# Optimization experiments

Measured on AMD Instinct MI355X. Metric: run time of the kernel, lower is better.

The kernel has to match this reference:

```python
import jax, jax.numpy as jnp
import numpy as np

B, T, N, L, D, F = 8, 1024, 512, 4096, 512, 64  # batch, target, nodes, leaves, d_model, d_feature
BR = L // N  # branching factor: leaves per node


def setup_inputs() -> dict:
    key = jax.random.key(0)
    ks = jax.random.split(key, 10)
    s = 0.02
    return {
        "root": jax.random.normal(ks[0], (B, 1, F), dtype=jnp.float32),
        "node": jax.random.normal(ks[1], (B, N, D), dtype=jnp.float32),
        "leaf": jax.random.normal(ks[2], (B, L, D), dtype=jnp.float32),
        "target": jax.random.normal(ks[3], (B, T, D), dtype=jnp.float32),
        "Wq": jax.random.normal(ks[4], (D, F), dtype=jnp.float32) * s,
        "bq": jnp.zeros((F,), dtype=jnp.float32),
        "Wk": jax.random.normal(ks[5], (D, F), dtype=jnp.float32) * s,
        "bk": jnp.zeros((F,), dtype=jnp.float32),
        "Wv": jax.random.normal(ks[6], (D, F), dtype=jnp.float32) * s,
        "bv": jnp.zeros((F,), dtype=jnp.float32),
        "Wagg": jax.random.normal(ks[7], (D, 1), dtype=jnp.float32) * s,
        "bagg": jnp.zeros((1,), dtype=jnp.float32),
    }


def reference(root, node, leaf, target, Wq, bq, Wk, bk, Wv, bv, Wagg, bagg):
    # Shared DecoderLinear projections (same weights used for node and leaf).
    q = target @ Wq + bq                      # [B,T,F]
    node_k = node @ Wk + bk                   # [B,N,F]
    node_v = node @ Wv + bv                   # [B,N,F]
    leaf_k = leaf @ Wk + bk                   # [B,L,F]
    leaf_v = leaf @ Wv + bv                   # [B,L,F]

    scale = 1.0 / jnp.sqrt(jnp.asarray(F, dtype=q.dtype))
    # Dual-key attention weights (no value-matmul inside attention()).
    Aqn = jax.nn.softmax(jnp.einsum('btf,bnf->btn', q, node_k) * scale, axis=-1)  # [B,T,N]
    Aql = jax.nn.softmax(jnp.einsum('btf,blf->btl', q, leaf_k) * scale, axis=-1)  # [B,T,L]

    # Tree interpolation: each leaf mixes root, its parent node value, and itself.
    node_rep = jnp.repeat(node_v, BR, axis=1)               # [B,L,F]
    interp = (root + node_rep + leaf_v) / 3.0               # [B,L,F]

    # Upward cumulative aggregation: suffix mean along the leaf dimension.
    rev_cumsum = jnp.cumsum(interp[:, ::-1, :], axis=1)[:, ::-1, :]  # [B,L,F]
    counts = (L - jnp.arange(L)).astype(interp.dtype)[None, :, None]
    upward = rev_cumsum / counts                                     # [B,L,F]

    # Weighted aggregation: learned softmax weights over each node's leaf group.
    w = jax.nn.softmax((leaf @ Wagg + bagg).reshape(B, N, BR), axis=-1)   # [B,N,BR]
    node_hat = jnp.einsum('bnc,bncf->bnf', w, upward.reshape(B, N, BR, F))  # [B,N,F]

    # Fused cat + matmul + softmax.
    A = jnp.concatenate([Aqn, Aql], axis=-1)          # [B,T,N+L]
    V = jnp.concatenate([node_hat, leaf_v], axis=-2)  # [B,N+L,F]
    return jax.nn.softmax(jnp.einsum('btm,bmf->btf', A, V), axis=-1)  # [B,T,F]
```

## Files before the change

kernel.cpp:

```cpp
#include <hip/hip_runtime.h>

#define B_ 8
#define T_ 1024
#define N_ 512
#define L_ 4096
#define D_ 512
#define F_ 64
#define SLICES 8
#define TPS 9
#define KSTR 72
#define XSTR 520

typedef __attribute__((ext_vector_type(8))) short short8;
typedef __attribute__((ext_vector_type(4))) float f32x4;

__device__ __forceinline__ unsigned short f2bf(float x){
    unsigned u = __builtin_bit_cast(unsigned, x);
    u += 0x7FFFu + ((u >> 16) & 1u);
    return (unsigned short)(u >> 16);
}
__device__ __forceinline__ unsigned pack_bf(float lo, float hi){
    return (unsigned)f2bf(lo) | ((unsigned)f2bf(hi) << 16);
}
__device__ __forceinline__ float bf2f(unsigned short s){
    return __builtin_bit_cast(float, ((unsigned)s) << 16);
}
__device__ __forceinline__ short8 frag_from4(unsigned d0, unsigned d1, unsigned d2, unsigned d3){
    union { unsigned u[4]; short8 s; } t;
    t.u[0] = d0; t.u[1] = d1; t.u[2] = d2; t.u[3] = d3;
    return t.s;
}

__global__ __launch_bounds__(64)
void prep_kernel(const float* __restrict__ Wq, const float* __restrict__ bq,
                 const float* __restrict__ Wk, const float* __restrict__ bk,
                 const float* __restrict__ Wv, const float* __restrict__ bv,
                 unsigned short* __restrict__ Wq_t, unsigned short* __restrict__ Wkv_t,
                 float* __restrict__ bq_s, float* __restrict__ bkv)
{
    const int n = blockIdx.x;
    const int lane = threadIdx.x;
    if (n == 192) {
        bq_s[lane]   = bq[lane] * 0.125f;
        bkv[lane]    = bk[lane];
        bkv[64+lane] = bv[lane];
        return;
    }
    const int d0 = lane * 8;
    unsigned short t[8];
    if (n < 64) {
        #pragma unroll
        for (int j = 0; j < 8; ++j) t[j] = f2bf(Wq[(size_t)(d0+j)*F_ + n] * 0.125f);
        *(uint4*)&Wq_t[(size_t)n*D_ + d0] = make_uint4(
            (unsigned)t[0]|((unsigned)t[1]<<16), (unsigned)t[2]|((unsigned)t[3]<<16),
            (unsigned)t[4]|((unsigned)t[5]<<16), (unsigned)t[6]|((unsigned)t[7]<<16));
    } else {
        const int nn  = n - 64;
        const float* W = (nn < 64) ? Wk : Wv;
        const int col = nn & 63;
        #pragma unroll
        for (int j = 0; j < 8; ++j) t[j] = f2bf(W[(size_t)(d0+j)*F_ + col]);
        *(uint4*)&Wkv_t[(size_t)nn*D_ + d0] = make_uint4(
            (unsigned)t[0]|((unsigned)t[1]<<16), (unsigned)t[2]|((unsigned)t[3]<<16),
            (unsigned)t[4]|((unsigned)t[5]<<16), (unsigned)t[6]|((unsigned)t[7]<<16));
    }
}

template<int MODE>
__device__ __forceinline__ void proj_body(
    int r0, unsigned short* Xs, unsigned short* Ws, unsigned short* Vt_lds,
    const float* __restrict__ X,
    const unsigned short* __restrict__ Wt,
    const float* __restrict__ bias,
    const float* __restrict__ Wagg, const float* __restrict__ bagg,
    unsigned short* __restrict__ outK, float* __restrict__ outVf,
    unsigned short* __restrict__ outVt, float* __restrict__ outAgg)
{
    constexpr int NPASS = (MODE == 0) ? 1 : 2;
    const int tid = threadIdx.x;
    const int l = tid & 63, c = l & 15, h = l >> 4;
    const int w  = tid >> 6;
    const int nt = w & 3;
    const int m  = w >> 2;

    const float4* xsrc = (const float4*)(X + (size_t)r0 * D_);
    #pragma unroll
    for (int j = 0; j < 8; ++j) {
        const int s = tid + j * 1024;
        const float4 v = xsrc[s];
        *(uint2*)&Xs[(s >> 7)*XSTR + (s & 127)*4] =
            make_uint2(pack_bf(v.x, v.y), pack_bf(v.z, v.w));
    }
    {
        const int r = tid >> 4, ch = tid & 15;
        const unsigned short* src = Wt + (size_t)r * D_ + ch*8;
        #pragma unroll
        for (int j = 0; j < 4; ++j)
            *(uint4*)&Ws[r*XSTR + ch*8 + j*128] = *(const uint4*)(src + j*128);
    }
    __syncthreads();

    #pragma unroll
    for (int p = 0; p < NPASS; ++p) {
        f32x4 acc = {0,0,0,0};
        #pragma unroll
        for (int kk = 0; kk < 16; ++kk) {
            const short8 bfr = *(const short8*)&Ws[(16*nt + c)*XSTR + kk*32 + 8*h];
            const short8 af  = *(const short8*)&Xs[(16*m  + c)*XSTR + kk*32 + 8*h];
            acc = __builtin_amdgcn_mfma_f32_16x16x32_bf16(af, bfr, acc, 0,0,0);
        }

        const float bc = bias[64*p + 16*nt + c];
        #pragma unroll
        for (int r = 0; r < 4; ++r) {
            const int row = r0 + 16*m + 4*h + r;
            const float v = acc[r] + bc;
            if (MODE == 0 || p == 0) {
                outK[(size_t)row*F_ + 16*nt + c] = f2bf(v);
            } else if (MODE == 1) {
                outVf[(size_t)row*F_ + 16*nt + c] = v;
            } else {
                Vt_lds[(16*nt + c)*72 + 16*m + 4*h + r] = f2bf(v);
            }
        }

        if (p + 1 < NPASS) {
            __syncthreads();
            const int r = tid >> 4, ch = tid & 15;
            const unsigned short* src = Wt + (size_t)(64 + r) * D_ + ch*8;
            #pragma unroll
            for (int j = 0; j < 4; ++j)
                *(uint4*)&Ws[r*XSTR + ch*8 + j*128] = *(const uint4*)(src + j*128);
            __syncthreads();
        }
    }

    if constexpr (MODE == 2) {
        __syncthreads();
        {
            const int row = tid >> 4, qd = tid & 15;
            const unsigned short* xr = &Xs[row*XSTR + qd*32];
            const float* wr = Wagg + qd*32;
            float pa = 0.f;
            #pragma unroll
            for (int j = 0; j < 4; ++j) {
                const short8 xv = *(const short8*)(xr + j*8);
                const float4 wa0 = *(const float4*)(wr + j*8);
                const float4 wa1 = *(const float4*)(wr + j*8 + 4);
                pa += bf2f((unsigned short)xv[0])*wa0.x + bf2f((unsigned short)xv[1])*wa0.y
                    + bf2f((unsigned short)xv[2])*wa0.z + bf2f((unsigned short)xv[3])*wa0.w
                    + bf2f((unsigned short)xv[4])*wa1.x + bf2f((unsigned short)xv[5])*wa1.y
                    + bf2f((unsigned short)xv[6])*wa1.z + bf2f((unsigned short)xv[7])*wa1.w;
            }
            pa += __shfl_xor(pa, 1);
            pa += __shfl_xor(pa, 2);
            pa += __shfl_xor(pa, 4);
            pa += __shfl_xor(pa, 8);
            if (qd == 0) outAgg[r0 + row] = pa + bagg[0];
        }
        {
            const int f = tid >> 4, seg = tid & 15;
            const int b = r0 >> 12, l0 = r0 & (L_ - 1);
            const uint2 a0 = *(const uint2*)&Vt_lds[f*72 + seg*4];
            *(uint2*)(outVt + ((size_t)(b*F_ + f))*L_ + l0 + seg*4) = a0;
        }
    }
}

__global__ __launch_bounds__(1024, 4)
void proj_all(const float* __restrict__ target, const float* __restrict__ node,
              const float* __restrict__ leaf,
              const unsigned short* __restrict__ Wq_t,
              const unsigned short* __restrict__ Wkv_t,
              const float* __restrict__ bq_s, const float* __restrict__ bkv,
              const float* __restrict__ Wagg, const float* __restrict__ bagg,
              unsigned short* __restrict__ q_bf, unsigned short* __restrict__ nk_bf,
              float* __restrict__ node_v, unsigned short* __restrict__ lk_bf,
              unsigned short* __restrict__ lvt, float* __restrict__ agg)
{
    __shared__ unsigned short Xs[64 * XSTR];
    __shared__ unsigned short Ws[64 * XSTR];
    __shared__ unsigned short Vt_lds[64 * 72];
    const int blk = blockIdx.x;
    if (blk < 512) {
        proj_body<2>(blk*64, Xs, Ws, Vt_lds, leaf, Wkv_t, bkv, Wagg, bagg,
                     lk_bf, nullptr, lvt, agg);
    } else if (blk < 640) {
        proj_body<0>((blk-512)*64, Xs, Ws, Vt_lds, target, Wq_t, bq_s, nullptr, nullptr,
                     q_bf, nullptr, nullptr, nullptr);
    } else {
        proj_body<1>((blk-640)*64, Xs, Ws, Vt_lds, node, Wkv_t, bkv, nullptr, nullptr,
                     nk_bf, node_v, nullptr, nullptr);
    }
}

__global__ __launch_bounds__(256)
void scan_nh_kernel(const unsigned short* __restrict__ lvt,
                    const float* __restrict__ node_v,
                    const float* __restrict__ root,
                    const float* __restrict__ agg,
                    unsigned short* __restrict__ nh_t)
{
    const int gtid = blockIdx.x * 256 + threadIdx.x;
    const int wv   = gtid >> 6;
    const int lane = threadIdx.x & 63;
    const int b = wv >> 6;
    const int f = wv & 63;

    const unsigned short* vt = lvt + ((size_t)(b*F_ + f))*L_ + lane*64;
    const float rootf = root[b*F_ + f];
    short8 xv[8]; float nv[8]; float gv[8];
    #pragma unroll
    for (int g = 0; g < 8; ++g) {
        xv[g] = *(const short8*)(vt + g*8);
        nv[g] = node_v[((size_t)(b*N_ + lane*8 + g))*F_ + f];
        float s8 = 0.f;
        #pragma unroll
        for (int j = 0; j < 8; ++j) s8 += bf2f((unsigned short)xv[g][j]);
        gv[g] = (s8 + 8.f*(rootf + nv[g])) * (1.f/3.f);
    }

    float s[9];
    s[8] = 0.f;
    #pragma unroll
    for (int j = 7; j >= 0; --j) s[j] = s[j+1] + gv[j];

    float x = s[0];
    const float lsum = x;
    #pragma unroll
    for (int off = 1; off < 64; off <<= 1) {
        float t = __shfl_down(x, off);
        if (lane + off < 64) x += t;
    }
    const float excl = x - lsum;

    const float* aggb = agg + (size_t)b*L_ + lane*64;
    unsigned short out8[8];
    #pragma unroll
    for (int g = 0; g < 8; ++g) {
        const float4 a0 = *(const float4*)(aggb + g*8);
        const float4 a1 = *(const float4*)(aggb + g*8 + 4);
        const float av[8] = {a0.x,a0.y,a0.z,a0.w, a1.x,a1.y,a1.z,a1.w};
        float mx = av[0];
        #pragma unroll
        for (int cc = 1; cc < 8; ++cc) mx = fmaxf(mx, av[cc]);
        float wgt[8]; float wsum = 0.f;
        #pragma unroll
        for (int cc = 0; cc < 8; ++cc) { wgt[cc] = __expf(av[cc] - mx); wsum += wgt[cc]; }

        const float tn = excl + s[g+1];
        float run = 0.f, acc = 0.f;
        #pragma unroll
        for (int cc = 7; cc >= 0; --cc) {
            const int ll = lane*64 + g*8 + cc;
            const float interp = (rootf + nv[g] + bf2f((unsigned short)xv[g][cc])) * (1.f/3.f);
            run += interp;
            const float up = (tn + run) / (float)(L_ - ll);
            acc = fmaf(wgt[cc], up, acc);
        }
        out8[g] = f2bf(acc / wsum);
    }
    *(uint4*)&nh_t[((size_t)(b*F_ + f))*N_ + lane*8] = *(const uint4*)out8;
}

__global__ __launch_bounds__(512, 4)
void attn_kernel(const unsigned short* __restrict__ qb,
                 const unsigned short* __restrict__ nk,
                 const unsigned short* __restrict__ nht,
                 const unsigned short* __restrict__ lk,
                 const unsigned short* __restrict__ lvt,
                 unsigned short* __restrict__ pacc, float* __restrict__ pd)
{
    __shared__ unsigned short Ks[2][64*KSTR];
    __shared__ unsigned short Vt[2][64*KSTR];

    const int wg  = (blockIdx.x & 7) * 64 + (blockIdx.x >> 3);
    const int b   = wg >> 6;
    const int sl  = (wg >> 3) & 7;
    const int t0  = (wg & 7) * 128;

    const int tid = threadIdx.x;
    const int w   = tid >> 6;
    const int l   = tid & 63;
    const int c   = l & 15;
    const int h   = l >> 4;
    const int sm  = tid >> 3;
    const int sc  = tid & 7;

    const unsigned short* qrow = qb + ((size_t)(b*T_ + t0 + w*16 + c))*F_ + 8*h;
    const short8 qf0 = *(const short8*)qrow;
    const short8 qf1 = *(const short8*)(qrow + 32);

    f32x4 accN[4] = {{0,0,0,0},{0,0,0,0},{0,0,0,0},{0,0,0,0}};
    f32x4 accL[4] = {{0,0,0,0},{0,0,0,0},{0,0,0,0},{0,0,0,0}};
    float dsN = 0.f, dsL = 0.f;

    const unsigned short* Knb = nk  + (size_t)b*N_*F_;
    const unsigned short* Klb = lk  + (size_t)b*L_*F_;
    const unsigned short* Vnb = nht + (size_t)b*F_*N_;
    const unsigned short* Vlb = lvt + (size_t)b*F_*L_;

    const int ti0 = sl * TPS;

    uint4 sk0, sv0;
    auto load_tile = [&](int ti) {
        if (ti < 8) {
            sk0 = *(const uint4*)(Knb + (size_t)ti*64*F_ + sm*64 + sc*8);
            sv0 = *(const uint4*)(Vnb + (size_t)sm*N_ + ti*64 + sc*8);
        } else {
            sk0 = *(const uint4*)(Klb + (size_t)(ti-8)*64*F_ + sm*64 + sc*8);
            sv0 = *(const uint4*)(Vlb + (size_t)sm*L_ + (ti-8)*64 + sc*8);
        }
    };
    auto write_tile = [&](int pb) {
        *(uint4*)&Ks[pb][sm*KSTR + sc*8] = sk0;
        *(uint4*)&Vt[pb][sm*KSTR + sc*8] = sv0;
    };

    load_tile(ti0);
    write_tile(0);
    __syncthreads();

    const int srcA = c + 16*((2*h) & 3);
    const int srcB = c + 16*((2*h + 1) & 3);
    const int hs   = h >> 1;

    for (int i = 0; i < TPS; ++i) {
        const int  ti  = ti0 + i;
        const bool isN = ti < 8;
        const int  pb  = i & 1;
        const bool nxt = (i + 1 < TPS);
        if (nxt) load_tile(ti + 1);

        f32x4 st[4] = {{0,0,0,0},{0,0,0,0},{0,0,0,0},{0,0,0,0}};
        #pragma unroll
        for (int ss = 0; ss < 4; ++ss) {
            const short8 kf0 = *(const short8*)&Ks[pb][(16*ss + c)*KSTR + 8*h];
            st[ss] = __builtin_amdgcn_mfma_f32_16x16x32_bf16(kf0, qf0, st[ss], 0,0,0);
            const short8 kf1 = *(const short8*)&Ks[pb][(16*ss + c)*KSTR + 32 + 8*h];
            st[ss] = __builtin_amdgcn_mfma_f32_16x16x32_bf16(kf1, qf1, st[ss], 0,0,0);
        }

        unsigned pk0[4], pk1[4];
        float psum = 0.f;
        #pragma unroll
        for (int ss = 0; ss < 4; ++ss) {
            #pragma unroll
            for (int r = 0; r < 4; ++r) { st[ss][r] = __expf(st[ss][r]); psum += st[ss][r]; }
            pk0[ss] = pack_bf(st[ss][0], st[ss][1]);
            pk1[ss] = pack_bf(st[ss][2], st[ss][3]);
        }
        if (isN) dsN += psum; else dsL += psum;

        #pragma unroll
        for (int k00 = 0; k00 < 2; ++k00) {
            const unsigned d0a = __shfl(pk0[2*k00+0], srcA);
            const unsigned d0b = __shfl(pk0[2*k00+1], srcA);
            const unsigned d1a = __shfl(pk1[2*k00+0], srcA);
            const unsigned d1b = __shfl(pk1[2*k00+1], srcA);
            const unsigned d2a = __shfl(pk0[2*k00+0], srcB);
            const unsigned d2b = __shfl(pk0[2*k00+1], srcB);
            const unsigned d3a = __shfl(pk1[2*k00+0], srcB);
            const unsigned d3b = __shfl(pk1[2*k00+1], srcB);
            const short8 bp = frag_from4(hs ? d0b : d0a, hs ? d1b : d1a,
                                         hs ? d2b : d2a, hs ? d3b : d3a);
            if (isN) {
                #pragma unroll
                for (int s2 = 0; s2 < 4; ++s2) {
                    const short8 af = *(const short8*)&Vt[pb][(16*s2 + c)*KSTR + 32*k00 + 8*h];
                    accN[s2] = __builtin_amdgcn_mfma_f32_16x16x32_bf16(af, bp, accN[s2], 0,0,0);
                }
            } else {
                #pragma unroll
                for (int s2 = 0; s2 < 4; ++s2) {
                    const short8 af = *(const short8*)&Vt[pb][(16*s2 + c)*KSTR + 32*k00 + 8*h];
                    accL[s2] = __builtin_amdgcn_mfma_f32_16x16x32_bf16(af, bp, accL[s2], 0,0,0);
                }
            }
        }

        if (nxt) {
            write_tile(pb ^ 1);
            __syncthreads();
        }
    }

    dsN += __shfl_xor(dsN, 16);  dsN += __shfl_xor(dsN, 32);
    dsL += __shfl_xor(dsL, 16);  dsL += __shfl_xor(dsL, 32);

    const int gt = b*T_ + t0 + w*16 + c;
    unsigned short* baseN = pacc + (((size_t)sl*(B_*T_) + gt)*2 + 0)*F_;
    unsigned short* baseL = baseN + F_;
    #pragma unroll
    for (int s2 = 0; s2 < 4; ++s2) {
        *(unsigned*)&baseN[s2*16 + 4*h]     = pack_bf(accN[s2][0], accN[s2][1]);
        *(unsigned*)&baseN[s2*16 + 4*h + 2] = pack_bf(accN[s2][2], accN[s2][3]);
        *(unsigned*)&baseL[s2*16 + 4*h]     = pack_bf(accL[s2][0], accL[s2][1]);
        *(unsigned*)&baseL[s2*16 + 4*h + 2] = pack_bf(accL[s2][2], accL[s2][3]);
    }
    if (h == 0) {
        pd[((size_t)sl*(B_*T_) + gt)*2 + 0] = dsN;
        pd[((size_t)sl*(B_*T_) + gt)*2 + 1] = dsL;
    }
}

__global__ __launch_bounds__(256)
void combine_kernel(const unsigned short* __restrict__ pacc,
                    const float* __restrict__ pd,
                    float* __restrict__ out)
{
    const int gt = (blockIdx.x * 256 + threadIdx.x) >> 6;
    const int f  = threadIdx.x & 63;

    float aN = 0.f, aL = 0.f, dN = 0.f, dL = 0.f;
    #pragma unroll
    for (int s = 0; s < SLICES; ++s) {
        const size_t base = ((size_t)s*(B_*T_) + gt)*2;
        aN += bf2f(pacc[(base + 0)*F_ + f]);
        aL += bf2f(pacc[(base + 1)*F_ + f]);
        dN += pd[base + 0];
        dL += pd[base + 1];
    }
    float lg = aN / dN + aL / dL;
    float mx = lg;
    #pragma unroll
    for (int off = 1; off < 64; off <<= 1) mx = fmaxf(mx, __shfl_xor(mx, off));
    const float e = __expf(lg - mx);
    float ssum = e;
    #pragma unroll
    for (int off = 1; off < 64; off <<= 1) ssum += __shfl_xor(ssum, off);
    out[(size_t)gt*F_ + f] = e / ssum;
}

extern "C" void kernel_launch(void* const* d_in, const int* in_sizes, int n_in,
                              void* d_out, int out_size, void* d_ws, size_t ws_size,
                              hipStream_t stream)
{
    const float* root   = (const float*)d_in[0];
    const float* node   = (const float*)d_in[1];
    const float* leaf   = (const float*)d_in[2];
    const float* target = (const float*)d_in[3];
    const float* Wq   = (const float*)d_in[4];
    const float* bq   = (const float*)d_in[5];
    const float* Wk   = (const float*)d_in[6];
    const float* bk   = (const float*)d_in[7];
    const float* Wv   = (const float*)d_in[8];
    const float* bv   = (const float*)d_in[9];
    const float* Wagg = (const float*)d_in[10];
    const float* bagg = (const float*)d_in[11];
    float* out = (float*)d_out;

    char* wp = (char*)d_ws;
    unsigned short* q_bf  = (unsigned short*)wp; wp += (size_t)B_*T_*F_*2;
    unsigned short* nk_bf = (unsigned short*)wp; wp += (size_t)B_*N_*F_*2;
    unsigned short* lk_bf = (unsigned short*)wp; wp += (size_t)B_*L_*F_*2;
    unsigned short* lvt   = (unsigned short*)wp; wp += (size_t)B_*F_*L_*2;
    unsigned short* nht   = (unsigned short*)wp; wp += (size_t)B_*F_*N_*2;
    unsigned short* Wq_t  = (unsigned short*)wp; wp += (size_t)64*D_*2;
    unsigned short* Wkv_t = (unsigned short*)wp; wp += (size_t)128*D_*2;
    float* node_v = (float*)wp; wp += (size_t)B_*N_*F_*4;
    float* agg    = (float*)wp; wp += (size_t)B_*L_*4;
    float* bq_s   = (float*)wp; wp += 512;
    float* bkv    = (float*)wp; wp += 512;
    unsigned short* pacc = (unsigned short*)wp; wp += (size_t)SLICES*B_*T_*2*F_*2;
    float* pd     = (float*)wp;

    prep_kernel<<<193, 64, 0, stream>>>(Wq, bq, Wk, bk, Wv, bv, Wq_t, Wkv_t, bq_s, bkv);
    proj_all<<<704, 1024, 0, stream>>>(target, node, leaf, Wq_t, Wkv_t, bq_s, bkv,
                                       Wagg, bagg, q_bf, nk_bf, node_v, lk_bf, lvt, agg);
    scan_nh_kernel<<<128, 256, 0, stream>>>(lvt, node_v, root, agg, nht);
    attn_kernel<<<B_*(T_/128)*SLICES, 512, 0, stream>>>(q_bf, nk_bf, nht, lk_bf, lvt, pacc, pd);
    combine_kernel<<<(B_*T_)/4, 256, 0, stream>>>(pacc, pd, out);
}
```

Before: 86.48 us.

## Split projection K-dimension into two halves to halve LDS and raise occupancy

The projection kernel now stages the 512-wide reduction dimension in two 256-wide chunks, shrinking the X and W LDS tiles from stride 520 to 264. Both K and V accumulators are kept live across chunks, and the aggregation dot product is accumulated per chunk. Launch bounds are raised from 4 to 8 blocks per CU so more blocks can be resident. The cost is extra barriers and reloading weight tiles per chunk, plus more register pressure from two live accumulators.

After: 78.78 us, median of 3. 8.9% less time.

```diff
diff --git a/kernel.cpp b/kernel.cpp
--- a/kernel.cpp
+++ b/kernel.cpp
@@ -9,7 +9,7 @@
 #define SLICES 8
 #define TPS 9
 #define KSTR 72
-#define XSTR 520
+#define XSTR 264
 
 typedef __attribute__((ext_vector_type(8))) short short8;
 typedef __attribute__((ext_vector_type(4))) float f32x4;
@@ -83,81 +83,107 @@
     const int nt = w & 3;
     const int m  = w >> 2;
 
-    const float4* xsrc = (const float4*)(X + (size_t)r0 * D_);
-    #pragma unroll
-    for (int j = 0; j < 8; ++j) {
-        const int s = tid + j * 1024;
-        const float4 v = xsrc[s];
-        *(uint2*)&Xs[(s >> 7)*XSTR + (s & 127)*4] =
-            make_uint2(pack_bf(v.x, v.y), pack_bf(v.z, v.w));
-    }
-    {
-        const int r = tid >> 4, ch = tid & 15;
-        const unsigned short* src = Wt + (size_t)r * D_ + ch*8;
-        #pragma unroll
-        for (int j = 0; j < 4; ++j)
-            *(uint4*)&Ws[r*XSTR + ch*8 + j*128] = *(const uint4*)(src + j*128);
-    }
-    __syncthreads();
-
-    #pragma unroll
-    for (int p = 0; p < NPASS; ++p) {
-        f32x4 acc = {0,0,0,0};
-        #pragma unroll
-        for (int kk = 0; kk < 16; ++kk) {
+    f32x4 acc0 = {0,0,0,0};
+    f32x4 acc1 = {0,0,0,0};
+    float pa = 0.f;
+
+    #pragma unroll
+    for (int kc = 0; kc < 2; ++kc) {
+        #pragma unroll
+        for (int j = 0; j < 4; ++j) {
+            const int s = tid + j * 1024;
+            const int row = s >> 6, col = s & 63;
+            const float4 v = *(const float4*)(X + (size_t)(r0+row)*D_ + kc*256 + col*4);
+            *(uint2*)&Xs[row*XSTR + col*4] =
+                make_uint2(pack_bf(v.x, v.y), pack_bf(v.z, v.w));
+        }
+        {
+            const int r = tid >> 4, ch = tid & 15;
+            #pragma unroll
+            for (int j = 0; j < 2; ++j) {
+                const int u = ch + j*16;
+                *(uint4*)&Ws[r*XSTR + u*8] =
+                    *(const uint4*)(Wt + (size_t)r*D_ + kc*256 + u*8);
+            }
+        }
+        __syncthreads();
+
+        #pragma unroll
+        for (int kk = 0; kk < 8; ++kk) {
             const short8 bfr = *(const short8*)&Ws[(16*nt + c)*XSTR + kk*32 + 8*h];
             const short8 af  = *(const short8*)&Xs[(16*m  + c)*XSTR + kk*32 + 8*h];
-            acc = __builtin_amdgcn_mfma_f32_16x16x32_bf16(af, bfr, acc, 0,0,0);
-        }
-
-        const float bc = bias[64*p + 16*nt + c];
+            acc0 = __builtin_amdgcn_mfma_f32_16x16x32_bf16(af, bfr, acc0, 0,0,0);
+        }
+        __syncthreads();
+
+        if constexpr (NPASS == 2) {
+            {
+                const int r = tid >> 4, ch = tid & 15;
+                #pragma unroll
+                for (int j = 0; j < 2; ++j) {
+                    const int u = ch + j*16;
+                    *(uint4*)&Ws[r*XSTR + u*8] =
+                        *(const uint4*)(Wt + (size_t)(64 + r)*D_ + kc*256 + u*8);
+                }
+            }
+            __syncthreads();
+            #pragma unroll
+            for (int kk = 0; kk < 8; ++kk) {
+                const short8 bfr = *(const short8*)&Ws[(16*nt + c)*XSTR + kk*32 + 8*h];
+                const short8 af  = *(const short8*)&Xs[(16*m  + c)*XSTR + kk*32 + 8*h];
+                acc1 = __builtin_amdgcn_mfma_f32_16x16x32_bf16(af, bfr, acc1, 0,0,0);
+            }
+            if constexpr (MODE == 2) {
+                const int row = tid >> 4, qd = tid & 15;
+                const unsigned short* xr = &Xs[row*XSTR + qd*16];
+                const float* wr = Wagg + kc*256 + qd*16;
+                #pragma unroll
+                for (int j = 0; j < 2; ++j) {
+                    const short8 xv = *(const short8*)(xr + j*8);
+                    const float4 wa0 = *(const float4*)(wr + j*8);
+                    const float4 wa1 = *(const float4*)(wr + j*8 + 4);
+                    pa += bf2f((unsigned short)xv[0])*wa0.x + bf2f((unsigned short)xv[1])*wa0.y
+                        + bf2f((unsigned short)xv[2])*wa0.z + bf2f((unsigned short)xv[3])*wa0.w
+                        + bf2f((unsigned short)xv[4])*wa1.x + bf2f((unsigned short)xv[5])*wa1.y
+                        + bf2f((unsigned short)xv[6])*wa1.z + bf2f((unsigned short)xv[7])*wa1.w;
+                }
+            }
+            __syncthreads();
+        }
+    }
+
+    {
+        const float bc0 = bias[16*nt + c];
         #pragma unroll
         for (int r = 0; r < 4; ++r) {
             const int row = r0 + 16*m + 4*h + r;
-            const float v = acc[r] + bc;
-            if (MODE == 0 || p == 0) {
-                outK[(size_t)row*F_ + 16*nt + c] = f2bf(v);
-            } else if (MODE == 1) {
+            outK[(size_t)row*F_ + 16*nt + c] = f2bf(acc0[r] + bc0);
+        }
+    }
+    if constexpr (NPASS == 2) {
+        const float bc1 = bias[64 + 16*nt + c];
+        #pragma unroll
+        for (int r = 0; r < 4; ++r) {
+            const int row = r0 + 16*m + 4*h + r;
+            const float v = acc1[r] + bc1;
+            if constexpr (MODE == 1) {
                 outVf[(size_t)row*F_ + 16*nt + c] = v;
             } else {
                 Vt_lds[(16*nt + c)*72 + 16*m + 4*h + r] = f2bf(v);
             }
         }
-
-        if (p + 1 < NPASS) {
-            __syncthreads();
-            const int r = tid >> 4, ch = tid & 15;
-            const unsigned short* src = Wt + (size_t)(64 + r) * D_ + ch*8;
-            #pragma unroll
-            for (int j = 0; j < 4; ++j)
-                *(uint4*)&Ws[r*XSTR + ch*8 + j*128] = *(const uint4*)(src + j*128);
-            __syncthreads();
-        }
     }
 
     if constexpr (MODE == 2) {
-        __syncthreads();
         {
             const int row = tid >> 4, qd = tid & 15;
-            const unsigned short* xr = &Xs[row*XSTR + qd*32];
-            const float* wr = Wagg + qd*32;
-            float pa = 0.f;
-            #pragma unroll
-            for (int j = 0; j < 4; ++j) {
-                const short8 xv = *(const short8*)(xr + j*8);
-                const float4 wa0 = *(const float4*)(wr + j*8);
-                const float4 wa1 = *(const float4*)(wr + j*8 + 4);
-                pa += bf2f((unsigned short)xv[0])*wa0.x + bf2f((unsigned short)xv[1])*wa0.y
-                    + bf2f((unsigned short)xv[2])*wa0.z + bf2f((unsigned short)xv[3])*wa0.w
-                    + bf2f((unsigned short)xv[4])*wa1.x + bf2f((unsigned short)xv[5])*wa1.y
-                    + bf2f((unsigned short)xv[6])*wa1.z + bf2f((unsigned short)xv[7])*wa1.w;
-            }
             pa += __shfl_xor(pa, 1);
             pa += __shfl_xor(pa, 2);
             pa += __shfl_xor(pa, 4);
             pa += __shfl_xor(pa, 8);
             if (qd == 0) outAgg[r0 + row] = pa + bagg[0];
         }
+        __syncthreads();
         {
             const int f = tid >> 4, seg = tid & 15;
             const int b = r0 >> 12, l0 = r0 & (L_ - 1);
@@ -167,7 +193,7 @@
     }
 }
 
-__global__ __launch_bounds__(1024, 4)
+__global__ __launch_bounds__(1024, 8)
 void proj_all(const float* __restrict__ target, const float* __restrict__ node,
               const float* __restrict__ leaf,
               const unsigned short* __restrict__ Wq_t,
```
